# Kernel optimization log

Measured on AMD Instinct MI355X. Metric: run time of the kernel, lower is better.

## Reference

```python
import jax, jax.numpy as jnp
import numpy as np


def setup_inputs() -> dict:
    key = jax.random.key(0)
    ks = jax.random.split(key, 6)
    B, S, AD, QD, A = 64, 2048, 1024, 1024, 1024
    scale = 0.02
    return {
        "input": jax.random.normal(ks[0], (B, QD), dtype=jnp.float32),
        "context": jax.random.normal(ks[1], (B, S, AD), dtype=jnp.float32),
        "W_pre": jax.random.normal(ks[2], (A, AD), dtype=jnp.float32) * scale,
        "b_pre": jax.random.normal(ks[3], (A,), dtype=jnp.float32) * scale,
        "W_q": jax.random.normal(ks[4], (A, QD), dtype=jnp.float32) * scale,
        "v": jax.random.normal(ks[5], (A,), dtype=jnp.float32) * scale,
    }


def reference(input, context, W_pre, b_pre, W_q, v):
    # precompute = linear_pre(context): [B, S, A]
    precompute = jnp.einsum("bsd,ad->bsa", context, W_pre) + b_pre
    # targetT = linear_q(input): [B, A], broadcast over sourceL
    targetT = jnp.einsum("bq,aq->ba", input, W_q)
    tmp = jnp.tanh(precompute + targetT[:, None, :])  # [B, S, A]
    energy = jnp.einsum("bsa,a->bs", tmp, v)          # linear_v, [B, S]
    score = jax.nn.softmax(energy, axis=1)             # softmax over sourceL
    weightedContext = jnp.einsum("bs,bsd->bd", score, context)
    return weightedContext, score, precompute
```

## Files before the change

kernel.cpp:

```cpp
#include <hip/hip_runtime.h>
#include <hip/hip_bf16.h>

#define BB   64
#define SS   2048
#define MM   (BB*SS)
#define NN   1024
#define KK   1024

typedef short bf16x8s __attribute__((ext_vector_type(8)));
typedef float f32x4   __attribute__((ext_vector_type(4)));

__device__ __forceinline__ short f2bf(float f) {
    union { __hip_bfloat16 h; short s; } u;
    u.h = __float2bfloat16(f);
    return u.s;
}

__device__ __forceinline__ bf16x8s cvt8(float4 a, float4 b) {
    bf16x8s r;
    r[0] = f2bf(a.x); r[1] = f2bf(a.y); r[2] = f2bf(a.z); r[3] = f2bf(a.w);
    r[4] = f2bf(b.x); r[5] = f2bf(b.y); r[6] = f2bf(b.z); r[7] = f2bf(b.w);
    return r;
}

__device__ __forceinline__ float tanh_fast(float x) {
    x = fminf(8.0f, fmaxf(-8.0f, x));
    float e = __expf(2.0f * x);
    return (e - 1.0f) / (e + 1.0f);
}

__device__ __forceinline__ void load_lds16(const void* g, void* l) {
    __builtin_amdgcn_global_load_lds(
        (const __attribute__((address_space(1))) unsigned int*)g,
        (__attribute__((address_space(3))) unsigned int*)l,
        16, 0, 0);
}

__global__ void cvt_bf16_kernel(const float* __restrict__ src,
                                __hip_bfloat16* __restrict__ dst, int n8) {
    int i = blockIdx.x * blockDim.x + threadIdx.x;
    const int stride = gridDim.x * blockDim.x;
    const float4* s4 = (const float4*)src;
    bf16x8s* d8 = (bf16x8s*)dst;
    for (; i < n8; i += stride) {
        d8[i] = cvt8(s4[i * 2], s4[i * 2 + 1]);
    }
}

__global__ void targetT_kernel(const float* __restrict__ input,
                               const float* __restrict__ W_q,
                               float* __restrict__ tgt) {
    __shared__ float inp[KK];
    const int t = threadIdx.x;
    const int b = blockIdx.x;
    const float* inRow = input + (size_t)b * KK;
    for (int i = t; i < KK; i += 256) inp[i] = inRow[i];
    __syncthreads();
    const int w = t >> 6, lane = t & 63;
    const int nbase = blockIdx.y * 256 + w * 64;
    for (int i = 0; i < 64; i++) {
        const int n = nbase + i;
        const float* wq = W_q + (size_t)n * KK;
        float a = 0.f;
        #pragma unroll
        for (int j = 0; j < 16; j++) a += wq[lane + 64 * j] * inp[lane + 64 * j];
        #pragma unroll
        for (int o = 32; o; o >>= 1) a += __shfl_xor(a, o);
        if (lane == 0) tgt[(size_t)b * NN + n] = a;
    }
}

__global__ __launch_bounds__(512, 2) void gemm8_kernel(
    const __hip_bfloat16* __restrict__ ctxb,
    const __hip_bfloat16* __restrict__ wpb,
    const float* __restrict__ bpre,
    const float* __restrict__ tgt,
    const float* __restrict__ vvec,
    float* __restrict__ pre,
    float* __restrict__ energy,
    int row0)
{
    __shared__ __align__(16) char lds[131072];

    const int nwg  = gridDim.x;
    const int orig = blockIdx.x;
    const int swz  = (orig & 7) * (nwg >> 3) + (orig >> 3);
    const int mTile = swz >> 2;
    const int nTile = swz & 3;
    const int blockM = mTile * 256;
    const int blockN = nTile * 256;

    const int t = threadIdx.x, w = t >> 6, lane = t & 63;
    const int wm = w >> 2, wn = w & 3;
    const int l15 = lane & 15;

    const int r0  = t >> 3;
    const int lc0 = ((t & 7) * 16) ^ ((r0 & 7) << 4);
    const char* aSrc = (const char*)ctxb + (size_t)(blockM + r0) * 2048 + lc0;
    const char* bSrc = (const char*)wpb  + (size_t)(blockN + r0) * 2048 + lc0;

#define STAGE_A(buf, half, T) do { \
    load_lds16(aSrc + (half)*262144 +          (T)*128, &lds[(buf)*32768 + (half)*16384 +        w*1024]); \
    load_lds16(aSrc + (half)*262144 + 131072 + (T)*128, &lds[(buf)*32768 + (half)*16384 + 8192 + w*1024]); \
} while(0)
#define STAGE_B(buf, half, T) do { \
    load_lds16(bSrc + (half)*262144 +          (T)*128, &lds[65536 + (buf)*32768 + (half)*16384 +        w*1024]); \
    load_lds16(bSrc + (half)*262144 + 131072 + (T)*128, &lds[65536 + (buf)*32768 + (half)*16384 + 8192 + w*1024]); \
} while(0)

    const int c16 = (lane >> 4) * 16;
    const int xo  = (lane & 7) << 4;
    const int bk0 = c16 ^ xo;
    const int bk1 = (64 + c16) ^ xo;
    const int aBase = wm * 16384 + l15 * 128;
    const int bBase = 65536 + wn * 8192 + l15 * 128;

    bf16x8s curA[4][2], B0f[2][2], B1f[2][2];

#define READ_A(buf, mbase) do { \
    _Pragma("unroll") \
    for (int mf = 0; mf < 4; mf++) { \
        curA[mf][0] = *(const bf16x8s*)&lds[(buf)*32768 + aBase + ((mbase)+mf)*2048 + bk0]; \
        curA[mf][1] = *(const bf16x8s*)&lds[(buf)*32768 + aBase + ((mbase)+mf)*2048 + bk1]; \
    } } while(0)
#define READ_B(dst, buf, nbase) do { \
    _Pragma("unroll") \
    for (int nf = 0; nf < 2; nf++) { \
        dst[nf][0] = *(const bf16x8s*)&lds[(buf)*32768 + bBase + ((nbase)+nf)*2048 + bk0]; \
        dst[nf][1] = *(const bf16x8s*)&lds[(buf)*32768 + bBase + ((nbase)+nf)*2048 + bk1]; \
    } } while(0)

    f32x4 acc[8][4];
    #pragma unroll
    for (int m = 0; m < 8; m++)
        #pragma unroll
        for (int n = 0; n < 4; n++)
            acc[m][n] = f32x4{0.f, 0.f, 0.f, 0.f};

#define MFMA_Q(mbase, B, nbase) do { \
    __builtin_amdgcn_s_setprio(1); \
    _Pragma("unroll") \
    for (int ks = 0; ks < 2; ks++) \
        _Pragma("unroll") \
        for (int mf = 0; mf < 4; mf++) \
            _Pragma("unroll") \
            for (int nf = 0; nf < 2; nf++) \
                acc[(mbase)+mf][(nbase)+nf] = __builtin_amdgcn_mfma_f32_16x16x32_bf16( \
                    curA[mf][ks], B[nf][ks], acc[(mbase)+mf][(nbase)+nf], 0, 0, 0); \
    __builtin_amdgcn_s_setprio(0); \
} while(0)

#define PH_MID() do { __builtin_amdgcn_s_barrier(); \
    asm volatile("s_waitcnt lgkmcnt(0)"); \
    __builtin_amdgcn_sched_barrier(0); } while(0)
#define PH_END() do { __builtin_amdgcn_sched_barrier(0); \
    __builtin_amdgcn_s_barrier(); } while(0)

    STAGE_B(0, 0, 0); STAGE_B(0, 1, 0);
    STAGE_A(0, 0, 0); STAGE_A(0, 1, 0);
    STAGE_B(1, 0, 1); STAGE_B(1, 1, 1);
    asm volatile("s_waitcnt vmcnt(4)");
    __builtin_amdgcn_sched_barrier(0);
    __builtin_amdgcn_s_barrier();

    #pragma unroll 1
    for (int i = 0; i < 8; i++) {
        const int Tn1 = 2 * i + 1;
        const int Tn2 = (2 * i + 2 > 15) ? 15 : 2 * i + 2;
        const int Tn3 = (2 * i + 3 > 15) ? 15 : 2 * i + 3;

        READ_A(0, 0); READ_B(B0f, 0, 0);
        STAGE_A(1, 0, Tn1);
        PH_MID(); MFMA_Q(0, B0f, 0); PH_END();
        READ_B(B1f, 0, 2);
        STAGE_A(1, 1, Tn1);
        PH_MID(); MFMA_Q(0, B1f, 2); PH_END();
        READ_A(0, 4);
        STAGE_B(0, 0, Tn2);
        PH_MID(); MFMA_Q(4, B0f, 0); PH_END();
        STAGE_B(0, 1, Tn2);
        PH_MID(); MFMA_Q(4, B1f, 2);
        asm volatile("s_waitcnt vmcnt(4)");
        PH_END();
        READ_A(1, 0); READ_B(B0f, 1, 0);
        STAGE_A(0, 0, Tn2);
        PH_MID(); MFMA_Q(0, B0f, 0); PH_END();
        READ_B(B1f, 1, 2);
        STAGE_A(0, 1, Tn2);
        PH_MID(); MFMA_Q(0, B1f, 2); PH_END();
        READ_A(1, 4);
        STAGE_B(1, 0, Tn3);
        PH_MID(); MFMA_Q(4, B0f, 0); PH_END();
        STAGE_B(1, 1, Tn3);
        PH_MID(); MFMA_Q(4, B1f, 2);
        asm volatile("s_waitcnt vmcnt(4)");
        PH_END();
    }

    asm volatile("s_waitcnt vmcnt(0)");

    const int bIdx = (row0 + blockM) >> 11;
    float bp[4], tq[4], vv[4];
    #pragma unroll
    for (int nf = 0; nf < 4; nf++) {
        const int col = blockN + wn * 64 + nf * 16 + l15;
        bp[nf] = bpre[col];
        tq[nf] = tgt[(size_t)bIdx * NN + col];
        vv[nf] = vvec[col];
    }
    const int gr0 = blockM + wm * 128 + ((lane >> 4) << 2);
    const int colBase = blockN + wn * 64 + l15;

    #pragma unroll
    for (int mf = 0; mf < 8; mf++) {
        #pragma unroll
        for (int j = 0; j < 4; j++) {
            const size_t rg = (size_t)row0 + gr0 + mf * 16 + j;
            float* prow = pre + rg * NN + colBase;
            float e = 0.f;
            #pragma unroll
            for (int nf = 0; nf < 4; nf++) {
                const float p = acc[mf][nf][j] + bp[nf];
                prow[nf * 16] = p;
                e += tanh_fast(p + tq[nf]) * vv[nf];
            }
            e += __shfl_xor(e, 1);
            e += __shfl_xor(e, 2);
            e += __shfl_xor(e, 4);
            e += __shfl_xor(e, 8);
            if (l15 == 0) atomicAdd(&energy[rg], e);
        }
    }
#undef STAGE_A
#undef STAGE_B
#undef READ_A
#undef READ_B
#undef MFMA_Q
#undef PH_MID
#undef PH_END
}

__global__ __launch_bounds__(256, 2) void gemm_energy_kernel(
    const float* __restrict__ ctx, const float* __restrict__ wpre,
    const float* __restrict__ bpre, const float* __restrict__ tgt,
    const float* __restrict__ vvec, float* __restrict__ pre,
    float* __restrict__ energy)
{
    __shared__ __align__(16) float As[128 * 32];
    __shared__ __align__(16) float Bs[128 * 32];

    const int orig = blockIdx.x;
    const int swz  = (orig & 7) * 1024 + (orig >> 3);
    const int mTile = swz >> 3;
    const int nTile = swz & 7;
    const size_t blockM = (size_t)mTile * 128;
    const int    blockN = nTile * 128;

    const int t = threadIdx.x, w = t >> 6, lane = t & 63;

    size_t aoff[4], boff[4];
    #pragma unroll
    for (int i = 0; i < 4; i++) {
        const int bb    = i * 4096 + w * 1024 + lane * 16;
        const int row   = bb >> 7;
        const int physc = bb & 127;
        const int logc  = physc ^ ((row & 7) << 4);
        aoff[i] = (blockM + (size_t)row) * (KK * 4) + logc;
        boff[i] = ((size_t)(blockN + row)) * (KK * 4) + logc;
    }
    const char* ctxB  = (const char*)ctx;
    const char* wpreB = (const char*)wpre;

    const int wm = (w >> 1) * 64, wn = (w & 1) * 64;

    int fa0[4], fa1[4], fb0[4], fb1[4];
    const int c0 = (lane >> 4) * 32;
    #pragma unroll
    for (int m = 0; m < 4; m++) {
        const int rA = wm + m * 16 + (lane & 15);
        const int sA = (rA & 7) << 4;
        fa0[m] = rA * 128 + (c0 ^ sA);
        fa1[m] = rA * 128 + ((c0 + 16) ^ sA);
        const int rB = wn + m * 16 + (lane & 15);
        const int sB = (rB & 7) << 4;
        fb0[m] = rB * 128 + (c0 ^ sB);
        fb1[m] = rB * 128 + ((c0 + 16) ^ sB);
    }

    f32x4 acc[4][4];
    #pragma unroll
    for (int m = 0; m < 4; m++)
        #pragma unroll
        for (int n = 0; n < 4; n++)
            acc[m][n] = f32x4{0.f, 0.f, 0.f, 0.f};

    for (int kt = 0; kt < KK / 32; kt++) {
        __syncthreads();
        #pragma unroll
        for (int i = 0; i < 4; i++) {
            load_lds16(ctxB  + aoff[i] + (size_t)kt * 128,
                       (char*)As + i * 4096 + w * 1024);
            load_lds16(wpreB + boff[i] + (size_t)kt * 128,
                       (char*)Bs + i * 4096 + w * 1024);
        }
        __syncthreads();

        bf16x8s af[4], bfr[4];
        #pragma unroll
        for (int m = 0; m < 4; m++) {
            float4 x0 = *(const float4*)((const char*)As + fa0[m]);
            float4 x1 = *(const float4*)((const char*)As + fa1[m]);
            af[m] = cvt8(x0, x1);
            float4 y0 = *(const float4*)((const char*)Bs + fb0[m]);
            float4 y1 = *(const float4*)((const char*)Bs + fb1[m]);
            bfr[m] = cvt8(y0, y1);
        }
        #pragma unroll
        for (int m = 0; m < 4; m++)
            #pragma unroll
            for (int n = 0; n < 4; n++)
                acc[m][n] = __builtin_amdgcn_mfma_f32_16x16x32_bf16(
                    af[m], bfr[n], acc[m][n], 0, 0, 0);
    }

    const int bIdx = (int)(blockM >> 11);
    float bp[4], tq[4], vv[4];
    #pragma unroll
    for (int n = 0; n < 4; n++) {
        const int col = blockN + wn + n * 16 + (lane & 15);
        bp[n] = bpre[col];
        tq[n] = tgt[(size_t)bIdx * NN + col];
        vv[n] = vvec[col];
    }
    const int colBase = blockN + wn + (lane & 15);

    #pragma unroll
    for (int m = 0; m < 4; m++) {
        const size_t rbase = blockM + wm + m * 16 + ((lane >> 4) << 2);
        #pragma unroll
        for (int j = 0; j < 4; j++) {
            const size_t rg = rbase + j;
            float* prow = pre + rg * NN + colBase;
            float e = 0.f;
            #pragma unroll
            for (int n = 0; n < 4; n++) {
                const float p = acc[m][n][j] + bp[n];
                prow[n * 16] = p;
                e += tanh_fast(p + tq[n]) * vv[n];
            }
            e += __shfl_xor(e, 1);
            e += __shfl_xor(e, 2);
            e += __shfl_xor(e, 4);
            e += __shfl_xor(e, 8);
            if ((lane & 15) == 0) atomicAdd(&energy[rg], e);
        }
    }
}

__global__ void softmax_kernel(const float* __restrict__ energy,
                               float* __restrict__ score) {
    const int b = blockIdx.x, t = threadIdx.x;
    const int w = t >> 6, lane = t & 63;
    const float4* e4 = (const float4*)(energy + (size_t)b * SS);
    float4 v0 = e4[t * 2], v1 = e4[t * 2 + 1];
    float x[8] = {v0.x, v0.y, v0.z, v0.w, v1.x, v1.y, v1.z, v1.w};

    float mx = x[0];
    #pragma unroll
    for (int i = 1; i < 8; i++) mx = fmaxf(mx, x[i]);
    #pragma unroll
    for (int o = 32; o; o >>= 1) mx = fmaxf(mx, __shfl_xor(mx, o));
    __shared__ float rmax[4], rsum[4];
    if (lane == 0) rmax[w] = mx;
    __syncthreads();
    mx = fmaxf(fmaxf(rmax[0], rmax[1]), fmaxf(rmax[2], rmax[3]));

    float s = 0.f;
    #pragma unroll
    for (int i = 0; i < 8; i++) { x[i] = __expf(x[i] - mx); s += x[i]; }
    #pragma unroll
    for (int o = 32; o; o >>= 1) s += __shfl_xor(s, o);
    if (lane == 0) rsum[w] = s;
    __syncthreads();
    s = rsum[0] + rsum[1] + rsum[2] + rsum[3];
    const float inv = 1.0f / s;

    float* sc = score + (size_t)b * SS + t * 8;
    #pragma unroll
    for (int i = 0; i < 8; i++) sc[i] = x[i] * inv;
}

__global__ void wctx_bf16_kernel(const __hip_bfloat16* __restrict__ ctxb,
                                 const float* __restrict__ score,
                                 float* __restrict__ wc) {
    const int b = blockIdx.x, scnk = blockIdx.y, t = threadIdx.x;
    __shared__ float ss[256];
    ss[t] = score[(size_t)b * SS + scnk * 256 + t];
    __syncthreads();
    const ushort4* cr = (const ushort4*)(ctxb + ((size_t)b * SS + (size_t)scnk * 256) * KK) + t;
    float4 a = {0.f, 0.f, 0.f, 0.f};
    #pragma unroll 4
    for (int s = 0; s < 256; s++) {
        const ushort4 c = cr[(size_t)s * 256];
        const float wgt = ss[s];
        a.x += wgt * __uint_as_float((unsigned)c.x << 16);
        a.y += wgt * __uint_as_float((unsigned)c.y << 16);
        a.z += wgt * __uint_as_float((unsigned)c.z << 16);
        a.w += wgt * __uint_as_float((unsigned)c.w << 16);
    }
    float* o = wc + (size_t)b * KK + t * 4;
    atomicAdd(o + 0, a.x);
    atomicAdd(o + 1, a.y);
    atomicAdd(o + 2, a.z);
    atomicAdd(o + 3, a.w);
}

__global__ void wctx_kernel(const float* __restrict__ ctx,
                            const float* __restrict__ score,
                            float* __restrict__ wc) {
    const int b = blockIdx.x, scnk = blockIdx.y, t = threadIdx.x;
    __shared__ float ss[256];
    ss[t] = score[(size_t)b * SS + scnk * 256 + t];
    __syncthreads();
    const float4* cr = (const float4*)(ctx + ((size_t)b * SS + (size_t)scnk * 256) * KK) + t;
    float4 a = {0.f, 0.f, 0.f, 0.f};
    #pragma unroll 4
    for (int s = 0; s < 256; s++) {
        const float4 c = cr[(size_t)s * 256];
        const float wgt = ss[s];
        a.x += wgt * c.x; a.y += wgt * c.y; a.z += wgt * c.z; a.w += wgt * c.w;
    }
    float* o = wc + (size_t)b * KK + t * 4;
    atomicAdd(o + 0, a.x);
    atomicAdd(o + 1, a.y);
    atomicAdd(o + 2, a.z);
    atomicAdd(o + 3, a.w);
}

extern "C" void kernel_launch(void* const* d_in, const int* in_sizes, int n_in,
                              void* d_out, int out_size, void* d_ws, size_t ws_size,
                              hipStream_t stream) {
    const float* input = (const float*)d_in[0];
    const float* ctx   = (const float*)d_in[1];
    const float* W_pre = (const float*)d_in[2];
    const float* b_pre = (const float*)d_in[3];
    const float* W_q   = (const float*)d_in[4];
    const float* v     = (const float*)d_in[5];

    float* out   = (float*)d_out;
    float* wc    = out;
    float* score = out + 65536;
    float* pre   = out + 65536 + 131072;

    float* tgt    = (float*)d_ws;
    float* energy = (float*)d_ws + 65536;
    __hip_bfloat16* wpb  = (__hip_bfloat16*)((char*)d_ws + 786432);
    __hip_bfloat16* ctxb = (__hip_bfloat16*)((char*)d_ws + 786432 + 2097152);

    long long avail = (long long)ws_size - 786432LL - 2097152LL;
    long long cr = avail > 0 ? (avail / (KK * 2)) : 0;
    cr &= ~511LL;
    int chunk_rows = (int)(cr > MM ? MM : cr);

    hipMemsetAsync(energy, 0, (size_t)MM * sizeof(float), stream);
    hipMemsetAsync(wc, 0, (size_t)BB * KK * sizeof(float), stream);

    targetT_kernel<<<dim3(BB, 4), 256, 0, stream>>>(input, W_q, tgt);

    if (chunk_rows >= 512) {
        cvt_bf16_kernel<<<512, 256, 0, stream>>>(W_pre, wpb, NN * KK / 8);
        for (int r0 = 0; r0 < MM; r0 += chunk_rows) {
            const int rows = (MM - r0) < chunk_rows ? (MM - r0) : chunk_rows;
            const int n8 = rows * KK / 8;
            const int cgrid = (n8 + 255) / 256 > 2048 ? 2048 : (n8 + 255) / 256;
            cvt_bf16_kernel<<<cgrid, 256, 0, stream>>>(
                ctx + (size_t)r0 * KK, ctxb, n8);
            gemm8_kernel<<<dim3((rows / 256) * 4), 512, 0, stream>>>(
                ctxb, wpb, b_pre, tgt, v, pre, energy, r0);
        }
    } else {
        gemm_energy_kernel<<<dim3((MM / 128) * (NN / 128)), 256, 0, stream>>>(
            ctx, W_pre, b_pre, tgt, v, pre, energy);
    }

    softmax_kernel<<<dim3(BB), 256, 0, stream>>>(energy, score);

    if (chunk_rows >= MM) {
        wctx_bf16_kernel<<<dim3(BB, 8), 256, 0, stream>>>(ctxb, score, wc);
    } else {
        wctx_kernel<<<dim3(BB, 8), 256, 0, stream>>>(ctx, score, wc);
    }
}
```

Measured before the change: 636.9 us.

## Replace energy atomics with per-N-tile partials and peel GEMM loop tail

Measured after the change: 620.3 us. 1.03x faster.

```diff
diff --git a/kernel.cpp b/kernel.cpp
--- a/kernel.cpp
+++ b/kernel.cpp
@@ -77,7 +77,7 @@
     const float* __restrict__ tgt,
     const float* __restrict__ vvec,
     float* __restrict__ pre,
-    float* __restrict__ energy,
+    float* __restrict__ energy4,
     int row0)
 {
     __shared__ __align__(16) char lds[131072];
@@ -150,25 +150,24 @@
     __builtin_amdgcn_s_setprio(0); \
 } while(0)
 
-#define PH_MID() do { __builtin_amdgcn_s_barrier(); \
+#define PH_MID() do { __builtin_amdgcn_sched_barrier(0); \
+    __builtin_amdgcn_s_barrier(); \
     asm volatile("s_waitcnt lgkmcnt(0)"); \
     __builtin_amdgcn_sched_barrier(0); } while(0)
 #define PH_END() do { __builtin_amdgcn_sched_barrier(0); \
     __builtin_amdgcn_s_barrier(); } while(0)
-
+#define VMCNT(n) do { asm volatile("s_waitcnt vmcnt(" #n ")"); \
+    __builtin_amdgcn_sched_barrier(0); } while(0)
+
+    STAGE_A(0, 0, 0); STAGE_A(0, 1, 0);
     STAGE_B(0, 0, 0); STAGE_B(0, 1, 0);
-    STAGE_A(0, 0, 0); STAGE_A(0, 1, 0);
     STAGE_B(1, 0, 1); STAGE_B(1, 1, 1);
-    asm volatile("s_waitcnt vmcnt(4)");
-    __builtin_amdgcn_sched_barrier(0);
+    VMCNT(4);
     __builtin_amdgcn_s_barrier();
 
     #pragma unroll 1
-    for (int i = 0; i < 8; i++) {
-        const int Tn1 = 2 * i + 1;
-        const int Tn2 = (2 * i + 2 > 15) ? 15 : 2 * i + 2;
-        const int Tn3 = (2 * i + 3 > 15) ? 15 : 2 * i + 3;
-
+    for (int i = 0; i < 7; i++) {
+        const int Tn1 = 2 * i + 1, Tn2 = 2 * i + 2, Tn3 = 2 * i + 3;
         READ_A(0, 0); READ_B(B0f, 0, 0);
         STAGE_A(1, 0, Tn1);
         PH_MID(); MFMA_Q(0, B0f, 0); PH_END();
@@ -180,7 +179,7 @@
         PH_MID(); MFMA_Q(4, B0f, 0); PH_END();
         STAGE_B(0, 1, Tn2);
         PH_MID(); MFMA_Q(4, B1f, 2);
-        asm volatile("s_waitcnt vmcnt(4)");
+        VMCNT(4);
         PH_END();
         READ_A(1, 0); READ_B(B0f, 1, 0);
         STAGE_A(0, 0, Tn2);
@@ -193,11 +192,28 @@
         PH_MID(); MFMA_Q(4, B0f, 0); PH_END();
         STAGE_B(1, 1, Tn3);
         PH_MID(); MFMA_Q(4, B1f, 2);
-        asm volatile("s_waitcnt vmcnt(4)");
+        VMCNT(4);
         PH_END();
     }
 
-    asm volatile("s_waitcnt vmcnt(0)");
+    READ_A(0, 0); READ_B(B0f, 0, 0);
+    STAGE_A(1, 0, 15);
+    PH_MID(); MFMA_Q(0, B0f, 0); PH_END();
+    READ_B(B1f, 0, 2);
+    STAGE_A(1, 1, 15);
+    PH_MID(); MFMA_Q(0, B1f, 2); PH_END();
+    READ_A(0, 4);
+    PH_MID(); MFMA_Q(4, B0f, 0); PH_END();
+    PH_MID(); MFMA_Q(4, B1f, 2);
+    VMCNT(0);
+    PH_END();
+    READ_A(1, 0); READ_B(B0f, 1, 0);
+    PH_MID(); MFMA_Q(0, B0f, 0); PH_END();
+    READ_B(B1f, 1, 2);
+    PH_MID(); MFMA_Q(0, B1f, 2); PH_END();
+    READ_A(1, 4);
+    PH_MID(); MFMA_Q(4, B0f, 0); PH_END();
+    PH_MID(); MFMA_Q(4, B1f, 2);
 
     const int bIdx = (row0 + blockM) >> 11;
     float bp[4], tq[4], vv[4];
@@ -210,6 +226,7 @@
     }
     const int gr0 = blockM + wm * 128 + ((lane >> 4) << 2);
     const int colBase = blockN + wn * 64 + l15;
+    float* epart = energy4 + (size_t)nTile * MM;
 
     #pragma unroll
     for (int mf = 0; mf < 8; mf++) {
@@ -228,7 +245,7 @@
             e += __shfl_xor(e, 2);
             e += __shfl_xor(e, 4);
             e += __shfl_xor(e, 8);
-            if (l15 == 0) atomicAdd(&energy[rg], e);
+            if (l15 == 0) epart[rg] = e;
         }
     }
 #undef STAGE_A
@@ -238,13 +255,14 @@
 #undef MFMA_Q
 #undef PH_MID
 #undef PH_END
+#undef VMCNT
 }
 
 __global__ __launch_bounds__(256, 2) void gemm_energy_kernel(
     const float* __restrict__ ctx, const float* __restrict__ wpre,
     const float* __restrict__ bpre, const float* __restrict__ tgt,
     const float* __restrict__ vvec, float* __restrict__ pre,
-    float* __restrict__ energy)
+    float* __restrict__ energy4)
 {
     __shared__ __align__(16) float As[128 * 32];
     __shared__ __align__(16) float Bs[128 * 32];
@@ -352,18 +370,24 @@
             e += __shfl_xor(e, 2);
             e += __shfl_xor(e, 4);
             e += __shfl_xor(e, 8);
-            if ((lane & 15) == 0) atomicAdd(&energy[rg], e);
+            if ((lane & 15) == 0) atomicAdd(&energy4[rg], e);
         }
     }
 }
 
-__global__ void softmax_kernel(const float* __restrict__ energy,
+__global__ void softmax_kernel(const float* __restrict__ energy4,
                                float* __restrict__ score) {
     const int b = blockIdx.x, t = threadIdx.x;
     const int w = t >> 6, lane = t & 63;
-    const float4* e4 = (const float4*)(energy + (size_t)b * SS);
-    float4 v0 = e4[t * 2], v1 = e4[t * 2 + 1];
-    float x[8] = {v0.x, v0.y, v0.z, v0.w, v1.x, v1.y, v1.z, v1.w};
+    const size_t base = (size_t)b * SS;
+    float x[8] = {0.f, 0.f, 0.f, 0.f, 0.f, 0.f, 0.f, 0.f};
+    #pragma unroll
+    for (int p = 0; p < 4; p++) {
+        const float4* e4 = (const float4*)(energy4 + (size_t)p * MM + base);
+        float4 v0 = e4[t * 2], v1 = e4[t * 2 + 1];
+        x[0] += v0.x; x[1] += v0.y; x[2] += v0.z; x[3] += v0.w;
+        x[4] += v1.x; x[5] += v1.y; x[6] += v1.z; x[7] += v1.w;
+    }
 
     float mx = x[0];
     #pragma unroll
@@ -385,7 +409,7 @@
     s = rsum[0] + rsum[1] + rsum[2] + rsum[3];
     const float inv = 1.0f / s;
 
-    float* sc = score + (size_t)b * SS + t * 8;
+    float* sc = score + base + t * 8;
     #pragma unroll
     for (int i = 0; i < 8; i++) sc[i] = x[i] * inv;
 }
@@ -452,17 +476,16 @@
     float* score = out + 65536;
     float* pre   = out + 65536 + 131072;
 
-    float* tgt    = (float*)d_ws;
-    float* energy = (float*)d_ws + 65536;
-    __hip_bfloat16* wpb  = (__hip_bfloat16*)((char*)d_ws + 786432);
-    __hip_bfloat16* ctxb = (__hip_bfloat16*)((char*)d_ws + 786432 + 2097152);
-
-    long long avail = (long long)ws_size - 786432LL - 2097152LL;
+    float* tgt     = (float*)d_ws;
+    float* energy4 = (float*)((char*)d_ws + 262144);
+    __hip_bfloat16* wpb  = (__hip_bfloat16*)((char*)d_ws + 262144 + 2097152);
+    __hip_bfloat16* ctxb = (__hip_bfloat16*)((char*)d_ws + 262144 + 2097152 + 2097152);
+
+    long long avail = (long long)ws_size - 262144LL - 2097152LL - 2097152LL;
     long long cr = avail > 0 ? (avail / (KK * 2)) : 0;
     cr &= ~511LL;
     int chunk_rows = (int)(cr > MM ? MM : cr);
 
-    hipMemsetAsync(energy, 0, (size_t)MM * sizeof(float), stream);
     hipMemsetAsync(wc, 0, (size_t)BB * KK * sizeof(float), stream);
 
     targetT_kernel<<<dim3(BB, 4), 256, 0, stream>>>(input, W_q, tgt);
@@ -472,18 +495,19 @@
         for (int r0 = 0; r0 < MM; r0 += chunk_rows) {
             const int rows = (MM - r0) < chunk_rows ? (MM - r0) : chunk_rows;
             const int n8 = rows * KK / 8;
-            const int cgrid = (n8 + 255) / 256 > 2048 ? 2048 : (n8 + 255) / 256;
+            const int cgrid = (n8 + 255) / 256 > 4096 ? 4096 : (n8 + 255) / 256;
             cvt_bf16_kernel<<<cgrid, 256, 0, stream>>>(
                 ctx + (size_t)r0 * KK, ctxb, n8);
             gemm8_kernel<<<dim3((rows / 256) * 4), 512, 0, stream>>>(
-                ctxb, wpb, b_pre, tgt, v, pre, energy, r0);
+                ctxb, wpb, b_pre, tgt, v, pre, energy4, r0);
         }
     } else {
+        hipMemsetAsync(energy4, 0, (size_t)4 * MM * sizeof(float), stream);
         gemm_energy_kernel<<<dim3((MM / 128) * (NN / 128)), 256, 0, stream>>>(
-            ctx, W_pre, b_pre, tgt, v, pre, energy);
-    }
-
-    softmax_kernel<<<dim3(BB), 256, 0, stream>>>(energy, score);
+            ctx, W_pre, b_pre, tgt, v, pre, energy4);
+    }
+
+    softmax_kernel<<<dim3(BB), 256, 0, stream>>>(energy4, score);
 
     if (chunk_rows >= MM) {
         wctx_bf16_kernel<<<dim3(BB, 8), 256, 0, stream>>>(ctxb, score, wc);
```
